# Kernel optimization log

Hardware: AMD Instinct MI355X
Metric: run time of the kernel (lower is better)

The kernel has to match this reference:

```python
import jax, jax.numpy as jnp
import numpy as np

NODES = 62        # electrodes per graph (hard-coded in model)
BATCH = 2048      # graphs per batch
N = NODES * BATCH # total nodes
IN = 128          # node feature dim (inchannel)
OUT = 62          # ChebConv out channels (hard-coded)
K = 3             # Chebyshev order (config.K)
LIN = 512         # linearsize
HC = 3            # classes (kwargs['HC'])
EPS = 1e-5        # BatchNorm eps
DEG = 4           # out-neighbors per node before symmetrization


def setup_inputs() -> dict:
    key = jax.random.key(0)
    ks = jax.random.split(key, 24)

    # Block-diagonal batched graph: same random 62-node topology per graph, offset per graph.
    rng = np.random.default_rng(0)
    src = np.repeat(np.arange(NODES), DEG)
    dst = (src + 1 + rng.integers(0, NODES - 1, size=src.shape)) % NODES  # no self-loops
    base = np.stack([np.concatenate([src, dst]), np.concatenate([dst, src])])  # [2, e] symmetric
    offs = (np.arange(BATCH) * NODES)[:, None, None]                            # [B,1,1]
    edge_index = (base[None] + offs).transpose(1, 0, 2).reshape(2, -1)          # [2, E]

    in_dims = [IN, IN + OUT, IN + 2 * OUT, IN + 3 * OUT]
    inp = {
        "x": jax.random.normal(ks[0], (N, IN), dtype=jnp.float32),
        "edge_index": jnp.asarray(edge_index, dtype=jnp.int32),
    }
    for i, d in enumerate(in_dims, start=1):
        inp[f"W{i}"] = jax.random.normal(ks[2 * i], (K, d, OUT), dtype=jnp.float32) * (1.0 / np.sqrt(d))
        inp[f"b{i}"] = jnp.zeros((OUT,), dtype=jnp.float32)
    feat = NODES * 4 * OUT  # 15376
    inp["Wh1"] = jax.random.normal(ks[10], (feat, LIN), dtype=jnp.float32) * (1.0 / np.sqrt(feat))
    inp["bh1"] = jnp.zeros((LIN,), dtype=jnp.float32)
    inp["g1"] = jnp.ones((LIN,), dtype=jnp.float32)
    inp["be1"] = jnp.zeros((LIN,), dtype=jnp.float32)
    inp["Wh2"] = jax.random.normal(ks[11], (LIN, LIN // 2), dtype=jnp.float32) * (1.0 / np.sqrt(LIN))
    inp["bh2"] = jnp.zeros((LIN // 2,), dtype=jnp.float32)
    inp["g2"] = jnp.ones((LIN // 2,), dtype=jnp.float32)
    inp["be2"] = jnp.zeros((LIN // 2,), dtype=jnp.float32)
    inp["Wh3"] = jax.random.normal(ks[12], (LIN // 2, HC), dtype=jnp.float32) * (1.0 / np.sqrt(LIN // 2))
    inp["bh3"] = jnp.zeros((HC,), dtype=jnp.float32)
    return inp


def _batchnorm(h, g, b):
    m = h.mean(axis=0)
    v = h.var(axis=0)  # biased, as torch BN training forward
    return (h - m) * jax.lax.rsqrt(v + EPS) * g + b


def reference(x, edge_index, W1, b1, W2, b2, W3, b3, W4, b4,
              Wh1, bh1, g1, be1, Wh2, bh2, g2, be2, Wh3, bh3):
    n = x.shape[0]
    row, col = edge_index[0], edge_index[1]

    # scaled Laplacian L~ = 2L/lambda_max - I = -D^{-1/2} A D^{-1/2} (sym norm, lambda_max=2)
    deg = jax.ops.segment_sum(jnp.ones(row.shape, x.dtype), row, num_segments=n)
    dinv = jnp.where(deg > 0, jnp.where(deg > 0, deg, 1.0) ** -0.5, 0.0)
    w = -(dinv[row] * dinv[col])  # [E]

    def prop(h):  # L~ @ h via edge scatter/gather
        return jax.ops.segment_sum(w[:, None] * h[col], row, num_segments=n)

    def cheb(h, W, b):  # sum_k T_k(L~) h @ W_k + b
        out = h @ W[0]
        Tx0, Tx1 = h, prop(h)
        out = out + Tx1 @ W[1]
        for k in range(2, W.shape[0]):
            Tx2 = 2.0 * prop(Tx1) - Tx0
            out = out + Tx2 @ W[k]
            Tx0, Tx1 = Tx1, Tx2
        return out + b

    relu = jax.nn.relu
    x1 = relu(cheb(x, W1, b1))
    x2 = relu(cheb(jnp.concatenate([x, x1], axis=1), W2, b2))
    x3 = relu(cheb(jnp.concatenate([x, x1, x2], axis=1), W3, b3))
    x4 = relu(cheb(jnp.concatenate([x, x1, x2, x3], axis=1), W4, b4))

    feats = jnp.concatenate([x1, x2, x3, x4], axis=1)        # [N, 4*OUT]
    feats = feats.reshape(BATCH, -1)                          # [B, 62*4*OUT] (attention==identity)

    h = relu(_batchnorm(feats @ Wh1 + bh1, g1, be1))          # dropout: identity (eval)
    h = relu(_batchnorm(h @ Wh2 + bh2, g2, be2))
    logits = h @ Wh3 + bh3
    return jax.nn.softmax(logits, axis=1)
```

## Files before the change

kernel.cpp:

```cpp
#include <hip/hip_runtime.h>


#define NODES   62
#define BATCH   2048
#define NTOT    (NODES * BATCH)
#define IN_DIM  128
#define OUT_DIM 62
#define ACOLS   248
#define FEAT    15376
#define LIN1    512
#define LIN2    256
#define NCLS    3
#define BN_EPS  1e-5f

typedef __attribute__((ext_vector_type(8)))  short  short8;
typedef __attribute__((ext_vector_type(4)))  float  f32x4;
typedef __attribute__((ext_vector_type(16))) float  f32x16;
typedef __attribute__((ext_vector_type(4)))  unsigned short us4;

__device__ inline unsigned short f2bf(float x) {
    unsigned u = __builtin_bit_cast(unsigned, x);
    return (unsigned short)((u + 0x7fffu + ((u >> 16) & 1u)) >> 16);
}
__device__ inline float bf2f(unsigned short h) {
    return __builtin_bit_cast(float, (unsigned)h << 16);
}
__device__ inline void tsplit(float x, unsigned short& hi, unsigned short& lo) {
    unsigned u = __builtin_bit_cast(unsigned, x);
    hi = (unsigned short)(u >> 16);
    float r = x - __builtin_bit_cast(float, u & 0xffff0000u);
    lo = (unsigned short)(__builtin_bit_cast(unsigned, r) >> 16);
}
__device__ inline int fo(int r, int k) {
    return (((r + 2 * k) & 15) + 16 * k) * 8;
}

#define PREP_GRID 11155
__global__ __launch_bounds__(256) void prep_kernel(
    const int* __restrict__ ei, int E, int epg, unsigned short* __restrict__ Tf,
    const float* __restrict__ W1, const float* __restrict__ W2,
    const float* __restrict__ W3, const float* __restrict__ W4,
    unsigned short* __restrict__ WTall,
    const float* __restrict__ Wh1, unsigned short* __restrict__ Wh1T,
    float* __restrict__ H1, const float* __restrict__ bh1,
    float* __restrict__ H2, const float* __restrict__ bh2,
    float* __restrict__ stats)
{
    __shared__ __align__(16) char ps[48640];
    const int bid = blockIdx.x;
    const int t   = threadIdx.x;

    if (bid == 0) {
        float* Ls   = (float*)ps;
        float* Ts   = (float*)(ps + 15376);
        int*   deg  = (int*)(ps + 48144);
        float* dinv = (float*)(ps + 48392);
        for (int i = t; i < NODES * NODES; i += 256) Ls[i] = 0.f;
        if (t < NODES) deg[t] = 0;
        __syncthreads();
        const int* row = ei;
        const int* col = ei + E;
        for (int j = t; j < epg; j += 256) atomicAdd(&deg[row[j]], 1);
        __syncthreads();
        if (t < NODES) dinv[t] = (deg[t] > 0) ? rsqrtf((float)deg[t]) : 0.f;
        __syncthreads();
        for (int j = t; j < epg; j += 256) {
            int r = row[j], c = col[j];
            atomicAdd(&Ls[r * NODES + c], -dinv[r] * dinv[c]);
        }
        __syncthreads();
        for (int idx = t; idx < 4096; idx += 256) {
            int r = idx >> 6, c = idx & 63;
            float t1 = 0.f, t2 = 0.f;
            if (r < NODES && c < NODES) {
                t1 = Ls[r * NODES + c];
                float s = 0.f;
                for (int j = 0; j < NODES; ++j) s += Ls[r * NODES + j] * Ls[j * NODES + c];
                t2 = 2.f * s - (r == c ? 1.f : 0.f);
            }
            Ts[idx]        = t1;
            Ts[4096 + idx] = t2;
        }
        __syncthreads();
        for (int idx = t; idx < 16384; idx += 256) {
            int j    = idx & 7;
            int lane = (idx >> 3) & 63;
            int pl   = (idx >> 9) & 1;
            int ks   = (idx >> 10) & 3;
            int w    = (idx >> 12) & 3;
            int m = (w & 1) * 32 + (lane & 31);
            int k = ks * 16 + (lane >> 5) * 8 + j;
            float v = Ts[(w >> 1) * 4096 + m * 64 + k];
            unsigned short hi, lo;
            tsplit(v, hi, lo);
            Tf[idx] = pl ? lo : hi;
        }
    } else if (bid < 1921) {
        const int li    = bid - 1;
        const int layer = li / 480;
        const int bx    = li - layer * 480;
        const float* W = (layer == 0) ? W1 : (layer == 1) ? W2 : (layer == 2) ? W3 : W4;
        const int d    = (layer == 0) ? 128 : (layer == 1) ? 190 : (layer == 2) ? 252 : 314;
        const int dpad = (layer == 0) ? 128 : (layer == 1) ? 192 : (layer == 2) ? 256 : 320;
        const int cum  = (layer == 0) ? 0 : (layer == 1) ? 4 : (layer == 2) ? 10 : 18;
        unsigned short* WTf = WTall + (size_t)cum * 12288;
        const int total = (dpad >> 5) * 12288;
        int idx = bx * 256 + t;
        if (idx >= total) return;
        int j    = idx & 7;
        int lane = (idx >> 3) & 63;
        int f    = idx >> 9;
        int nt   = f & 1;
        int pl   = (f >> 1) & 1;
        int ks   = (f >> 2) & 1;
        int seg  = (f >> 3) % 3;
        int ch   = (f >> 3) / 3;
        int n  = nt * 32 + (lane & 31);
        int kk = ch * 32 + ks * 16 + (lane >> 5) * 8 + j;
        float v = (n < NODES && kk < d) ? W[((size_t)seg * d + kk) * OUT_DIM + n] : 0.f;
        unsigned short hi, lo;
        tsplit(v, hi, lo);
        WTf[idx] = pl ? lo : hi;
    } else if (bid < 9617) {
        const int ti = bid - 1921;
        const int k0 = (ti % 481) * 32;
        const int n0 = (ti / 481) * 32;
        float (*T)[33] = (float(*)[33])ps;
        {
            int kl = t >> 3, n4 = (t & 7) * 4;
            if (k0 + kl < FEAT) {
                float4 v = *(const float4*)&Wh1[(size_t)(k0 + kl) * LIN1 + n0 + n4];
                T[kl][n4] = v.x; T[kl][n4 + 1] = v.y; T[kl][n4 + 2] = v.z; T[kl][n4 + 3] = v.w;
            }
        }
        __syncthreads();
        {
            int nl = t >> 3, k4 = (t & 7) * 4;
            if (k0 + k4 + 3 < FEAT) {
                ushort4 o;
                o.x = f2bf(T[k4 + 0][nl]);
                o.y = f2bf(T[k4 + 1][nl]);
                o.z = f2bf(T[k4 + 2][nl]);
                o.w = f2bf(T[k4 + 3][nl]);
                *(ushort4*)&Wh1T[(size_t)(n0 + nl) * FEAT + k0 + k4] = o;
            }
        }
    } else {
        const int i = (bid - 9617) * 256 + t;
        const int n1 = BATCH * LIN1 / 4;
        const int n2 = BATCH * LIN2 / 4;
        if (i < n1) {
            ((float4*)H1)[i] = ((const float4*)bh1)[i & (LIN1 / 4 - 1)];
        } else if (i - n1 < n2) {
            int j = i - n1;
            ((float4*)H2)[j] = ((const float4*)bh2)[j & (LIN2 / 4 - 1)];
        } else {
            int j = i - n1 - n2;
            if (j < 512)
                ((float4*)stats)[j] = (float4){0.f, 0.f, 0.f, 0.f};
        }
    }
}

__global__ __launch_bounds__(256, 4) void cheb_mfma(
    const float* __restrict__ x, float* __restrict__ X248,
    const unsigned short* __restrict__ WTf, const unsigned short* __restrict__ Tf,
    const float* __restrict__ bias, int d, int dpad)
{
    __shared__ __align__(16) unsigned short smem[17408];
    __shared__ float bias_s[64];

    unsigned short* hA = smem;
    unsigned short* Bs = smem + 5120;

    const int tid  = threadIdx.x;
    const int g    = blockIdx.x;
    const int lane = tid & 63;
    const int wv   = tid >> 6;
    const int mtw  = wv >> 1, ntw = wv & 1;

    if (tid < 64) bias_s[tid] = (tid < OUT_DIM) ? bias[tid] : 0.f;

    const int srow = tid >> 2;
    const int scg  = (tid & 3) * 8;

    const int nchunk = dpad >> 5;

    f32x16 acc[3];
    #pragma unroll
    for (int s = 0; s < 3; ++s)
        #pragma unroll
        for (int i = 0; i < 16; ++i) acc[s][i] = 0.f;

    float  vh[8];
    short8 breg[6];

#define LOADCH(cn)                                                             \
    do {                                                                       \
        const int gf_ = (cn) * 32 + scg;                                       \
        if (srow < NODES) {                                                    \
            if ((cn) * 32 < IN_DIM) {                                          \
                const float4* p_ = (const float4*)&x[(size_t)(g * NODES + srow) * IN_DIM + gf_]; \
                float4 a_ = p_[0], b_ = p_[1];                                 \
                vh[0] = a_.x; vh[1] = a_.y; vh[2] = a_.z; vh[3] = a_.w;        \
                vh[4] = b_.x; vh[5] = b_.y; vh[6] = b_.z; vh[7] = b_.w;        \
            } else if (gf_ + 8 <= d) {                                         \
                const float4* p_ = (const float4*)&X248[(size_t)(g * NODES + srow) * ACOLS + (gf_ - IN_DIM)]; \
                float4 a_ = p_[0], b_ = p_[1];                                 \
                vh[0] = a_.x; vh[1] = a_.y; vh[2] = a_.z; vh[3] = a_.w;        \
                vh[4] = b_.x; vh[5] = b_.y; vh[6] = b_.z; vh[7] = b_.w;        \
            } else {                                                           \
                _Pragma("unroll")                                              \
                for (int p = 0; p < 8; ++p)                                    \
                    vh[p] = (gf_ + p < d)                                      \
                        ? X248[(size_t)(g * NODES + srow) * ACOLS + (gf_ - IN_DIM) + p] : 0.f; \
            }                                                                  \
        } else {                                                               \
            _Pragma("unroll")                                                  \
            for (int p = 0; p < 8; ++p) vh[p] = 0.f;                           \
        }                                                                      \
        const short8* wsrc_ = (const short8*)(WTf + (size_t)(cn) * 12288);     \
        _Pragma("unroll")                                                      \
        for (int i = 0; i < 6; ++i) breg[i] = wsrc_[i * 256 + tid];            \
    } while (0)

    LOADCH(0);

    for (int ch = 0; ch < nchunk; ++ch) {
        {
            short8 hi8, lo8;
            #pragma unroll
            for (int p = 0; p < 8; ++p) {
                unsigned short h_, l_;
                tsplit(vh[p], h_, l_);
                hi8[p] = (short)h_; lo8[p] = (short)l_;
            }
            *(short8*)&hA[srow * 40 + scg]        = hi8;
            *(short8*)&hA[2560 + srow * 40 + scg] = lo8;
            #pragma unroll
            for (int i = 0; i < 6; ++i) ((short8*)Bs)[i * 256 + tid] = breg[i];
        }
        __syncthreads();
        if (ch + 1 < nchunk) LOADCH(ch + 1);
        {
            const int arow = mtw * 32 + (lane & 31);
            const int akf  = (lane >> 5) * 8;
            #pragma unroll
            for (int ks = 0; ks < 2; ++ks) {
                short8 ahi = *(const short8*)&hA[arow * 40 + ks * 16 + akf];
                short8 alo = *(const short8*)&hA[2560 + arow * 40 + ks * 16 + akf];
                #pragma unroll
                for (int seg = 0; seg < 3; ++seg) {
                    const unsigned short* bp =
                        Bs + ((((seg * 2 + ks) * 2 + 0) * 2 + ntw) << 9) + lane * 8;
                    short8 bhi = *(const short8*)bp;
                    short8 blo = *(const short8*)(bp + 1024);
                    acc[seg] = __builtin_amdgcn_mfma_f32_32x32x16_bf16(ahi, bhi, acc[seg], 0, 0, 0);
                    acc[seg] = __builtin_amdgcn_mfma_f32_32x32x16_bf16(ahi, blo, acc[seg], 0, 0, 0);
                    acc[seg] = __builtin_amdgcn_mfma_f32_32x32x16_bf16(alo, bhi, acc[seg], 0, 0, 0);
                }
            }
        }
        __syncthreads();
    }
#undef LOADCH

    short8 Tr[2][4][2];
    #pragma unroll
    for (int mat = 0; mat < 2; ++mat) {
        const int w = mat * 2 + mtw;
        #pragma unroll
        for (int ks = 0; ks < 4; ++ks)
            #pragma unroll
            for (int pl = 0; pl < 2; ++pl)
                Tr[mat][ks][pl] =
                    *(const short8*)(Tf + (((size_t)(w * 4 + ks) * 2 + pl) << 9) + lane * 8);
    }
    {
        const int jb = (lane >> 5) * 4;
        const int lq = lane & 31;
        #pragma unroll
        for (int q = 0; q < 4; ++q) {
            const int ks2 = mtw * 2 + (q >> 1);
            const int lp  = lq + 32 * (q & 1);
            us4 s1h, s1l, s2h, s2l;
            #pragma unroll
            for (int r = 0; r < 4; ++r) {
                unsigned short hi_, lo_;
                tsplit(acc[1][q * 4 + r], hi_, lo_);
                s1h[r] = hi_; s1l[r] = lo_;
                tsplit(acc[2][q * 4 + r], hi_, lo_);
                s2h[r] = hi_; s2l[r] = lo_;
            }
            const int base = lp * 8 + jb;
            *(us4*)&smem[((((0 + ks2) * 2 + 0) * 2 + ntw) << 9) + base] = s1h;
            *(us4*)&smem[((((0 + ks2) * 2 + 1) * 2 + ntw) << 9) + base] = s1l;
            *(us4*)&smem[((((4 + ks2) * 2 + 0) * 2 + ntw) << 9) + base] = s2h;
            *(us4*)&smem[((((4 + ks2) * 2 + 1) * 2 + ntw) << 9) + base] = s2l;
        }
    }
    __syncthreads();
    f32x16 out = acc[0];
    #pragma unroll
    for (int mat = 0; mat < 2; ++mat)
        #pragma unroll
        for (int ks = 0; ks < 4; ++ks) {
            const unsigned short* sp =
                smem + ((((mat * 4 + ks) * 2 + 0) * 2 + ntw) << 9) + lane * 8;
            short8 shi = *(const short8*)sp;
            short8 slo = *(const short8*)(sp + 1024);
            out = __builtin_amdgcn_mfma_f32_32x32x16_bf16(Tr[mat][ks][0], shi, out, 0, 0, 0);
            out = __builtin_amdgcn_mfma_f32_32x32x16_bf16(Tr[mat][ks][0], slo, out, 0, 0, 0);
            out = __builtin_amdgcn_mfma_f32_32x32x16_bf16(Tr[mat][ks][1], shi, out, 0, 0, 0);
        }
    {
        const int c = ntw * 32 + (lane & 31);
        if (c < OUT_DIM) {
            const int mbase = mtw * 32 + 4 * (lane >> 5);
            #pragma unroll
            for (int reg = 0; reg < 16; ++reg) {
                int m = mbase + (reg & 3) + 8 * (reg >> 2);
                if (m < NODES) {
                    float v = fmaxf(out[reg] + bias_s[c], 0.f);
                    X248[(size_t)(g * NODES + m) * ACOLS + (d - IN_DIM) + c] = v;
                }
            }
        }
    }
}

#define SPLIT1 8
__global__ __launch_bounds__(256) void gemm_head1_mfma(
    const float* __restrict__ F32, const unsigned short* __restrict__ WT1,
    float* __restrict__ H1)
{
    __shared__ __align__(16) unsigned short A16[4 * 512];
    __shared__ __align__(16) unsigned short B16[8 * 512];
    const int tid  = threadIdx.x;
    const int lane = tid & 63;
    const int wv   = tid >> 6;
    const int bm = blockIdx.x, bnb = blockIdx.y, s = blockIdx.z;
    const int c0 = (481 * s) / SPLIT1, c1 = (481 * (s + 1)) / SPLIT1;
    const int mr = tid >> 2, kg = (tid & 3) * 8;
    const int mrB = tid >> 1, kgB = (tid & 1) * 16;
    const int aoff  = (mr >> 4) * 512 + fo(mr & 15, tid & 3);
    const int boff0 = (mrB >> 4) * 512 + fo(mrB & 15, (tid & 1) * 2);
    const int boff1 = (mrB >> 4) * 512 + fo(mrB & 15, (tid & 1) * 2 + 1);
    const int roff  = fo(lane & 15, lane >> 4);

    f32x4 acc[8];
    #pragma unroll
    for (int i = 0; i < 8; ++i) acc[i] = (f32x4){0.f, 0.f, 0.f, 0.f};

    float4 u0, u1;
    short8 bv0, bv1;
#define LOAD1(cn)                                                              \
    do {                                                                       \
        const int k_ = (cn) * 32 + kg;                                         \
        u0 = (float4){0.f, 0.f, 0.f, 0.f};                                     \
        u1 = (float4){0.f, 0.f, 0.f, 0.f};                                     \
        bv0 = (short8){0, 0, 0, 0, 0, 0, 0, 0};                                \
        bv1 = (short8){0, 0, 0, 0, 0, 0, 0, 0};                                \
        if (k_ + 8 <= FEAT) {                                                  \
            const float4* p_ = (const float4*)&F32[(size_t)(bm * 64 + mr) * FEAT + k_]; \
            u0 = p_[0]; u1 = p_[1];                                            \
        }                                                                      \
        const int kB_ = (cn) * 32 + kgB;                                       \
        if (kB_ + 8 <= FEAT)                                                   \
            bv0 = *(const short8*)&WT1[(size_t)(bnb * 128 + mrB) * FEAT + kB_]; \
        if (kB_ + 16 <= FEAT)                                                  \
            bv1 = *(const short8*)&WT1[(size_t)(bnb * 128 + mrB) * FEAT + kB_ + 8]; \
    } while (0)

    LOAD1(c0);
    for (int ch = c0; ch < c1; ++ch) {
        {
            short8 av;
            av[0] = (short)f2bf(u0.x); av[1] = (short)f2bf(u0.y);
            av[2] = (short)f2bf(u0.z); av[3] = (short)f2bf(u0.w);
            av[4] = (short)f2bf(u1.x); av[5] = (short)f2bf(u1.y);
            av[6] = (short)f2bf(u1.z); av[7] = (short)f2bf(u1.w);
            *(short8*)&A16[aoff]  = av;
            *(short8*)&B16[boff0] = bv0;
            *(short8*)&B16[boff1] = bv1;
        }
        __syncthreads();
        if (ch + 1 < c1) LOAD1(ch + 1);
        short8 af = *(short8*)&A16[wv * 512 + roff];
        #pragma unroll
        for (int nt = 0; nt < 8; ++nt) {
            short8 bf = *(short8*)&B16[nt * 512 + roff];
            acc[nt] = __builtin_amdgcn_mfma_f32_16x16x32_bf16(af, bf, acc[nt], 0, 0, 0);
        }
        __syncthreads();
    }
#undef LOAD1
    const int m0 = bm * 64 + wv * 16 + (lane >> 4) * 4;
    #pragma unroll
    for (int nt = 0; nt < 8; ++nt) {
        int c = bnb * 128 + nt * 16 + (lane & 15);
        #pragma unroll
        for (int rg = 0; rg < 4; ++rg)
            atomicAdd(&H1[(size_t)(m0 + rg) * LIN1 + c], acc[nt][rg]);
    }
}

__global__ __launch_bounds__(256) void bn_stats(
    const float* __restrict__ H, int C,
    float* __restrict__ Sg, float* __restrict__ S2g)
{
    const int ct = threadIdx.x & 15;
    const int rt = threadIdx.x >> 4;
    const int c  = blockIdx.x * 16 + ct;
    const int r0 = blockIdx.y * 16 + rt;
    float s = 0.f, s2 = 0.f;
    for (int r = r0; r < BATCH; r += 256) {
        float v = H[(size_t)r * C + c];
        s += v; s2 += v * v;
    }
    __shared__ float Ss[16][17], S2s[16][17];
    Ss[rt][ct] = s; S2s[rt][ct] = s2;
    __syncthreads();
    if (rt == 0) {
        float ts = 0.f, ts2 = 0.f;
        #pragma unroll
        for (int i = 0; i < 16; ++i) { ts += Ss[i][ct]; ts2 += S2s[i][ct]; }
        atomicAdd(&Sg[c], ts);
        atomicAdd(&S2g[c], ts2);
    }
}

#define ACC16(av, bv) do {                              \
    acc[0][0] = fmaf((av).x, (bv).x, acc[0][0]);        \
    acc[0][1] = fmaf((av).x, (bv).y, acc[0][1]);        \
    acc[0][2] = fmaf((av).x, (bv).z, acc[0][2]);        \
    acc[0][3] = fmaf((av).x, (bv).w, acc[0][3]);        \
    acc[1][0] = fmaf((av).y, (bv).x, acc[1][0]);        \
    acc[1][1] = fmaf((av).y, (bv).y, acc[1][1]);        \
    acc[1][2] = fmaf((av).y, (bv).z, acc[1][2]);        \
    acc[1][3] = fmaf((av).y, (bv).w, acc[1][3]);        \
    acc[2][0] = fmaf((av).z, (bv).x, acc[2][0]);        \
    acc[2][1] = fmaf((av).z, (bv).y, acc[2][1]);        \
    acc[2][2] = fmaf((av).z, (bv).z, acc[2][2]);        \
    acc[2][3] = fmaf((av).z, (bv).w, acc[2][3]);        \
    acc[3][0] = fmaf((av).w, (bv).x, acc[3][0]);        \
    acc[3][1] = fmaf((av).w, (bv).y, acc[3][1]);        \
    acc[3][2] = fmaf((av).w, (bv).z, acc[3][2]);        \
    acc[3][3] = fmaf((av).w, (bv).w, acc[3][3]);        \
} while (0)

#define SPLIT2 4
__global__ __launch_bounds__(256) void gemm2_kernel(
    const float* __restrict__ A, const float* __restrict__ B,
    float* __restrict__ C,
    const float* __restrict__ Sg1, const float* __restrict__ S2g1,
    const float* __restrict__ g1, const float* __restrict__ be1)
{
    __shared__ __align__(16) float As[16 * 72];
    __shared__ __align__(16) float Bs[16 * 64];
    __shared__ float scs[128], shs[128];
    const int bm = blockIdx.x, bnb = blockIdx.y, s = blockIdx.z;
    const int tid = threadIdx.x;
    const int ty4 = (tid >> 4) * 4;
    const int tx4 = (tid & 15) * 4;
    const int kbeg = s * (LIN1 / SPLIT2);
    const int kend = kbeg + LIN1 / SPLIT2;
    if (tid < 128) {
        const int k = kbeg + tid;
        float mn  = Sg1[k] * (1.f / BATCH);
        float var = S2g1[k] * (1.f / BATCH) - mn * mn;
        float sc  = g1[k] * rsqrtf(var + BN_EPS);
        scs[tid] = sc;
        shs[tid] = be1[k] - mn * sc;
    }
    __syncthreads();
    float acc[4][4] = {};
    for (int k0 = kbeg; k0 < kend; k0 += 16) {
        for (int i = tid; i < 1024; i += 256) {
            int m = i >> 4, kt = i & 15;
            float raw = A[(size_t)(bm * 64 + m) * LIN1 + k0 + kt];
            int kl = k0 + kt - kbeg;
            As[kt * 72 + m] = fmaxf(fmaf(raw, scs[kl], shs[kl]), 0.f);
        }
        for (int i = tid; i < 1024; i += 256) {
            int kt = i >> 6, c = i & 63;
            Bs[kt * 64 + c] = B[(size_t)(k0 + kt) * LIN2 + bnb * 64 + c];
        }
        __syncthreads();
        #pragma unroll
        for (int kt = 0; kt < 16; ++kt) {
            const float4 av = *(const float4*)&As[kt * 72 + ty4];
            const float4 bv = *(const float4*)&Bs[kt * 64 + tx4];
            ACC16(av, bv);
        }
        __syncthreads();
    }
    const int b = bm * 64 + ty4, c = bnb * 64 + tx4;
    #pragma unroll
    for (int i = 0; i < 4; ++i)
        #pragma unroll
        for (int j = 0; j < 4; ++j)
            atomicAdd(&C[(size_t)(b + i) * LIN2 + c + j], acc[i][j]);
}

__global__ __launch_bounds__(256) void final_kernel(
    const float* __restrict__ H2, const float* __restrict__ Wh3,
    const float* __restrict__ bh3, float* __restrict__ out,
    const float* __restrict__ Sg2, const float* __restrict__ S2g2,
    const float* __restrict__ g2, const float* __restrict__ be2)
{
    __shared__ float Ws[LIN2 * NCLS];
    __shared__ float bs[NCLS];
    __shared__ float sc2[LIN2], sh2[LIN2];
    const int tid = threadIdx.x;
    for (int i = tid; i < LIN2 * NCLS; i += 256) Ws[i] = Wh3[i];
    if (tid < NCLS) bs[tid] = bh3[tid];
    {
        float mn  = Sg2[tid] * (1.f / BATCH);
        float var = S2g2[tid] * (1.f / BATCH) - mn * mn;
        float sc  = g2[tid] * rsqrtf(var + BN_EPS);
        sc2[tid] = sc;
        sh2[tid] = be2[tid] - mn * sc;
    }
    __syncthreads();
    const int r     = blockIdx.x * 32 + (tid >> 3);
    const int lane8 = tid & 7;
    float a0 = (lane8 == 0) ? bs[0] : 0.f;
    float a1 = (lane8 == 0) ? bs[1] : 0.f;
    float a2 = (lane8 == 0) ? bs[2] : 0.f;
    const float4* row = (const float4*)&H2[(size_t)r * LIN2];
    #pragma unroll
    for (int i = 0; i < 8; ++i) {
        const int k4 = lane8 + i * 8;
        float4 h = row[k4];
        const int k = k4 * 4;
        float h0 = fmaxf(fmaf(h.x, sc2[k + 0], sh2[k + 0]), 0.f);
        float h1 = fmaxf(fmaf(h.y, sc2[k + 1], sh2[k + 1]), 0.f);
        float h2v = fmaxf(fmaf(h.z, sc2[k + 2], sh2[k + 2]), 0.f);
        float h3 = fmaxf(fmaf(h.w, sc2[k + 3], sh2[k + 3]), 0.f);
        a0 = fmaf(h0, Ws[(k + 0) * 3 + 0], a0);
        a1 = fmaf(h0, Ws[(k + 0) * 3 + 1], a1);
        a2 = fmaf(h0, Ws[(k + 0) * 3 + 2], a2);
        a0 = fmaf(h1, Ws[(k + 1) * 3 + 0], a0);
        a1 = fmaf(h1, Ws[(k + 1) * 3 + 1], a1);
        a2 = fmaf(h1, Ws[(k + 1) * 3 + 2], a2);
        a0 = fmaf(h2v, Ws[(k + 2) * 3 + 0], a0);
        a1 = fmaf(h2v, Ws[(k + 2) * 3 + 1], a1);
        a2 = fmaf(h2v, Ws[(k + 2) * 3 + 2], a2);
        a0 = fmaf(h3, Ws[(k + 3) * 3 + 0], a0);
        a1 = fmaf(h3, Ws[(k + 3) * 3 + 1], a1);
        a2 = fmaf(h3, Ws[(k + 3) * 3 + 2], a2);
    }
    #pragma unroll
    for (int m = 1; m < 8; m <<= 1) {
        a0 += __shfl_xor(a0, m);
        a1 += __shfl_xor(a1, m);
        a2 += __shfl_xor(a2, m);
    }
    if (lane8 == 0) {
        float mx = fmaxf(a0, fmaxf(a1, a2));
        float e0 = expf(a0 - mx), e1 = expf(a1 - mx), e2 = expf(a2 - mx);
        float inv = 1.f / (e0 + e1 + e2);
        out[r * 3 + 0] = e0 * inv;
        out[r * 3 + 1] = e1 * inv;
        out[r * 3 + 2] = e2 * inv;
    }
}

extern "C" void kernel_launch(void* const* d_in, const int* in_sizes, int n_in,
                              void* d_out, int out_size, void* d_ws, size_t ws_size,
                              hipStream_t stream)
{
    const float* x   = (const float*)d_in[0];
    const int*   ei  = (const int*)  d_in[1];
    const float* W1  = (const float*)d_in[2];
    const float* b1  = (const float*)d_in[3];
    const float* W2  = (const float*)d_in[4];
    const float* b2  = (const float*)d_in[5];
    const float* W3  = (const float*)d_in[6];
    const float* b3  = (const float*)d_in[7];
    const float* W4  = (const float*)d_in[8];
    const float* b4  = (const float*)d_in[9];
    const float* Wh1 = (const float*)d_in[10];
    const float* bh1 = (const float*)d_in[11];
    const float* g1  = (const float*)d_in[12];
    const float* be1 = (const float*)d_in[13];
    const float* Wh2 = (const float*)d_in[14];
    const float* bh2 = (const float*)d_in[15];
    const float* g2  = (const float*)d_in[16];
    const float* be2 = (const float*)d_in[17];
    const float* Wh3 = (const float*)d_in[18];
    const float* bh3 = (const float*)d_in[19];
    float* out = (float*)d_out;

    char* ws = (char*)d_ws;
    float* Sg1  = (float*)(ws + 0);
    float* S2g1 = (float*)(ws + 2048);
    float* Sg2  = (float*)(ws + 4096);
    float* S2g2 = (float*)(ws + 5120);
    unsigned short* Tf    = (unsigned short*)(ws + 32768);
    unsigned short* WTall = (unsigned short*)(ws + 65536);
    unsigned short* Wh1T  = (unsigned short*)(ws + 753664);
    float* X248 = (float*)(ws + 16498688);
    float* H1   = (float*)(ws + 142458880);
    float* H2   = (float*)(ws + 146653184);

    const int E   = in_sizes[1] / 2;
    const int epg = E / BATCH;

    prep_kernel<<<PREP_GRID, 256, 0, stream>>>(
        ei, E, epg, Tf, W1, W2, W3, W4, WTall, Wh1, Wh1T, H1, bh1, H2, bh2,
        (float*)ws);

    cheb_mfma<<<BATCH, 256, 0, stream>>>(x, X248, WTall + (size_t)0 * 12288,  Tf, b1, 128, 128);
    cheb_mfma<<<BATCH, 256, 0, stream>>>(x, X248, WTall + (size_t)4 * 12288,  Tf, b2, 190, 192);
    cheb_mfma<<<BATCH, 256, 0, stream>>>(x, X248, WTall + (size_t)10 * 12288, Tf, b3, 252, 256);
    cheb_mfma<<<BATCH, 256, 0, stream>>>(x, X248, WTall + (size_t)18 * 12288, Tf, b4, 314, 320);

    gemm_head1_mfma<<<dim3(32, 4, SPLIT1), 256, 0, stream>>>(X248, Wh1T, H1);

    bn_stats<<<dim3(LIN1 / 16, 16), 256, 0, stream>>>(H1, LIN1, Sg1, S2g1);
    gemm2_kernel<<<dim3(32, 4, SPLIT2), 256, 0, stream>>>(H1, Wh2, H2, Sg1, S2g1, g1, be1);
    bn_stats<<<dim3(LIN2 / 16, 16), 256, 0, stream>>>(H2, LIN2, Sg2, S2g2);
    final_kernel<<<BATCH / 32, 256, 0, stream>>>(H2, Wh3, bh3, out, Sg2, S2g2, g2, be2);
}
```

Baseline: 518.8 us.

## Store Cheb outputs as pre-split bf16 hi/lo and fold head prep into layer-1 launch

Cheb layer outputs are now stored as bf16 hi/lo pairs (round-to-nearest split) instead of fp32. Later layers therefore load pre-split values without re-splitting, and the head GEMM reads the bf16 hi half directly with no per-chunk conversion. The Wh1 transpose/convert and H1/H2/stats initialisation move out of the prep kernel into extra blocks of the first cheb launch, so they overlap with layer-1 compute. This trades extra index arithmetic and a changed rounding scheme for less memory traffic and less conversion work.

```diff
diff --git a/kernel.cpp b/kernel.cpp
--- a/kernel.cpp
+++ b/kernel.cpp
@@ -8,6 +8,7 @@
 #define OUT_DIM 62
 #define ACOLS   248
 #define FEAT    15376
+#define GSTR    30752
 #define LIN1    512
 #define LIN2    256
 #define NCLS    3
@@ -31,20 +32,20 @@
     float r = x - __builtin_bit_cast(float, u & 0xffff0000u);
     lo = (unsigned short)(__builtin_bit_cast(unsigned, r) >> 16);
 }
+__device__ inline void rsplit(float x, unsigned short& hi, unsigned short& lo) {
+    hi = f2bf(x);
+    lo = f2bf(x - bf2f(hi));
+}
 __device__ inline int fo(int r, int k) {
     return (((r + 2 * k) & 15) + 16 * k) * 8;
 }
 
-#define PREP_GRID 11155
-__global__ __launch_bounds__(256) void prep_kernel(
+#define PREPC_GRID 1921
+__global__ __launch_bounds__(256) void prep_core(
     const int* __restrict__ ei, int E, int epg, unsigned short* __restrict__ Tf,
     const float* __restrict__ W1, const float* __restrict__ W2,
     const float* __restrict__ W3, const float* __restrict__ W4,
-    unsigned short* __restrict__ WTall,
-    const float* __restrict__ Wh1, unsigned short* __restrict__ Wh1T,
-    float* __restrict__ H1, const float* __restrict__ bh1,
-    float* __restrict__ H2, const float* __restrict__ bh2,
-    float* __restrict__ stats)
+    unsigned short* __restrict__ WTall)
 {
     __shared__ __align__(16) char ps[48640];
     const int bid = blockIdx.x;
@@ -95,7 +96,7 @@
             tsplit(v, hi, lo);
             Tf[idx] = pl ? lo : hi;
         }
-    } else if (bid < 1921) {
+    } else {
         const int li    = bid - 1;
         const int layer = li / 480;
         const int bx    = li - layer * 480;
@@ -121,60 +122,71 @@
         unsigned short hi, lo;
         tsplit(v, hi, lo);
         WTf[idx] = pl ? lo : hi;
-    } else if (bid < 9617) {
-        const int ti = bid - 1921;
-        const int k0 = (ti % 481) * 32;
-        const int n0 = (ti / 481) * 32;
-        float (*T)[33] = (float(*)[33])ps;
-        {
-            int kl = t >> 3, n4 = (t & 7) * 4;
-            if (k0 + kl < FEAT) {
-                float4 v = *(const float4*)&Wh1[(size_t)(k0 + kl) * LIN1 + n0 + n4];
-                T[kl][n4] = v.x; T[kl][n4 + 1] = v.y; T[kl][n4 + 2] = v.z; T[kl][n4 + 3] = v.w;
-            }
-        }
-        __syncthreads();
-        {
-            int nl = t >> 3, k4 = (t & 7) * 4;
-            if (k0 + k4 + 3 < FEAT) {
-                ushort4 o;
-                o.x = f2bf(T[k4 + 0][nl]);
-                o.y = f2bf(T[k4 + 1][nl]);
-                o.z = f2bf(T[k4 + 2][nl]);
-                o.w = f2bf(T[k4 + 3][nl]);
-                *(ushort4*)&Wh1T[(size_t)(n0 + nl) * FEAT + k0 + k4] = o;
-            }
-        }
-    } else {
-        const int i = (bid - 9617) * 256 + t;
-        const int n1 = BATCH * LIN1 / 4;
-        const int n2 = BATCH * LIN2 / 4;
-        if (i < n1) {
-            ((float4*)H1)[i] = ((const float4*)bh1)[i & (LIN1 / 4 - 1)];
-        } else if (i - n1 < n2) {
-            int j = i - n1;
-            ((float4*)H2)[j] = ((const float4*)bh2)[j & (LIN2 / 4 - 1)];
-        } else {
-            int j = i - n1 - n2;
-            if (j < 512)
-                ((float4*)stats)[j] = (float4){0.f, 0.f, 0.f, 0.f};
-        }
     }
 }
 
 __global__ __launch_bounds__(256, 4) void cheb_mfma(
-    const float* __restrict__ x, float* __restrict__ X248,
+    const float* __restrict__ x, unsigned short* __restrict__ Xs,
     const unsigned short* __restrict__ WTf, const unsigned short* __restrict__ Tf,
-    const float* __restrict__ bias, int d, int dpad)
+    const float* __restrict__ bias, int d, int dpad,
+    const float* __restrict__ Wh1, unsigned short* __restrict__ Wh1T,
+    float* __restrict__ H1, const float* __restrict__ bh1,
+    float* __restrict__ H2, const float* __restrict__ bh2,
+    float* __restrict__ stats)
 {
     __shared__ __align__(16) unsigned short smem[17408];
     __shared__ float bias_s[64];
 
+    const int bid = blockIdx.x;
+    const int tid = threadIdx.x;
+
+    if (bid >= BATCH) {
+        const int j = bid - BATCH;
+        if (j < 7696) {
+            const int k0 = (j % 481) * 32;
+            const int n0 = (j / 481) * 32;
+            float (*T)[33] = (float(*)[33])smem;
+            {
+                int kl = tid >> 3, n4 = (tid & 7) * 4;
+                if (k0 + kl < FEAT) {
+                    float4 v = *(const float4*)&Wh1[(size_t)(k0 + kl) * LIN1 + n0 + n4];
+                    T[kl][n4] = v.x; T[kl][n4 + 1] = v.y; T[kl][n4 + 2] = v.z; T[kl][n4 + 3] = v.w;
+                }
+            }
+            __syncthreads();
+            {
+                int nl = tid >> 3, k4 = (tid & 7) * 4;
+                if (k0 + k4 + 3 < FEAT) {
+                    ushort4 o;
+                    o.x = f2bf(T[k4 + 0][nl]);
+                    o.y = f2bf(T[k4 + 1][nl]);
+                    o.z = f2bf(T[k4 + 2][nl]);
+                    o.w = f2bf(T[k4 + 3][nl]);
+                    *(ushort4*)&Wh1T[(size_t)(n0 + nl) * FEAT + k0 + k4] = o;
+                }
+            }
+        } else {
+            const int i = (j - 7696) * 256 + tid;
+            const int n1 = BATCH * LIN1 / 4;
+            const int n2 = BATCH * LIN2 / 4;
+            if (i < n1) {
+                ((float4*)H1)[i] = ((const float4*)bh1)[i & (LIN1 / 4 - 1)];
+            } else if (i - n1 < n2) {
+                int jj = i - n1;
+                ((float4*)H2)[jj] = ((const float4*)bh2)[jj & (LIN2 / 4 - 1)];
+            } else {
+                int jj = i - n1 - n2;
+                if (jj < 512)
+                    ((float4*)stats)[jj] = (float4){0.f, 0.f, 0.f, 0.f};
+            }
+        }
+        return;
+    }
+
     unsigned short* hA = smem;
     unsigned short* Bs = smem + 5120;
 
-    const int tid  = threadIdx.x;
-    const int g    = blockIdx.x;
+    const int g    = bid;
     const int lane = tid & 63;
     const int wv   = tid >> 6;
     const int mtw  = wv >> 1, ntw = wv & 1;
@@ -183,6 +195,7 @@
 
     const int srow = tid >> 2;
     const int scg  = (tid & 3) * 8;
+    const size_t xbh = (size_t)g * GSTR + (size_t)srow * ACOLS;
 
     const int nchunk = dpad >> 5;
 
@@ -193,31 +206,37 @@
         for (int i = 0; i < 16; ++i) acc[s][i] = 0.f;
 
     float  vh[8];
+    short8 hv, lv;
     short8 breg[6];
 
 #define LOADCH(cn)                                                             \
     do {                                                                       \
         const int gf_ = (cn) * 32 + scg;                                       \
         if (srow < NODES) {                                                    \
-            if ((cn) * 32 < IN_DIM) {                                          \
+            if ((cn) < 4) {                                                    \
                 const float4* p_ = (const float4*)&x[(size_t)(g * NODES + srow) * IN_DIM + gf_]; \
                 float4 a_ = p_[0], b_ = p_[1];                                 \
                 vh[0] = a_.x; vh[1] = a_.y; vh[2] = a_.z; vh[3] = a_.w;        \
                 vh[4] = b_.x; vh[5] = b_.y; vh[6] = b_.z; vh[7] = b_.w;        \
             } else if (gf_ + 8 <= d) {                                         \
-                const float4* p_ = (const float4*)&X248[(size_t)(g * NODES + srow) * ACOLS + (gf_ - IN_DIM)]; \
-                float4 a_ = p_[0], b_ = p_[1];                                 \
-                vh[0] = a_.x; vh[1] = a_.y; vh[2] = a_.z; vh[3] = a_.w;        \
-                vh[4] = b_.x; vh[5] = b_.y; vh[6] = b_.z; vh[7] = b_.w;        \
+                hv = *(const short8*)&Xs[xbh + (gf_ - IN_DIM)];                \
+                lv = *(const short8*)&Xs[xbh + FEAT + (gf_ - IN_DIM)];         \
             } else {                                                           \
                 _Pragma("unroll")                                              \
-                for (int p = 0; p < 8; ++p)                                    \
-                    vh[p] = (gf_ + p < d)                                      \
-                        ? X248[(size_t)(g * NODES + srow) * ACOLS + (gf_ - IN_DIM) + p] : 0.f; \
+                for (int p = 0; p < 8; ++p) {                                  \
+                    const int gfp = gf_ + p;                                   \
+                    hv[p] = (gfp < d) ? (short)Xs[xbh + (gfp - IN_DIM)] : (short)0; \
+                    lv[p] = (gfp < d) ? (short)Xs[xbh + FEAT + (gfp - IN_DIM)] : (short)0; \
+                }                                                              \
             }                                                                  \
         } else {                                                               \
-            _Pragma("unroll")                                                  \
-            for (int p = 0; p < 8; ++p) vh[p] = 0.f;                           \
+            if ((cn) < 4) {                                                    \
+                _Pragma("unroll")                                              \
+                for (int p = 0; p < 8; ++p) vh[p] = 0.f;                       \
+            } else {                                                           \
+                hv = (short8){0, 0, 0, 0, 0, 0, 0, 0};                         \
+                lv = (short8){0, 0, 0, 0, 0, 0, 0, 0};                         \
+            }                                                                  \
         }                                                                      \
         const short8* wsrc_ = (const short8*)(WTf + (size_t)(cn) * 12288);     \
         _Pragma("unroll")                                                      \
@@ -229,11 +248,15 @@
     for (int ch = 0; ch < nchunk; ++ch) {
         {
             short8 hi8, lo8;
-            #pragma unroll
-            for (int p = 0; p < 8; ++p) {
-                unsigned short h_, l_;
-                tsplit(vh[p], h_, l_);
-                hi8[p] = (short)h_; lo8[p] = (short)l_;
+            if (ch < 4) {
+                #pragma unroll
+                for (int p = 0; p < 8; ++p) {
+                    unsigned short h_, l_;
+                    rsplit(vh[p], h_, l_);
+                    hi8[p] = (short)h_; lo8[p] = (short)l_;
+                }
+            } else {
+                hi8 = hv; lo8 = lv;
             }
             *(short8*)&hA[srow * 40 + scg]        = hi8;
             *(short8*)&hA[2560 + srow * 40 + scg] = lo8;
@@ -300,7 +323,7 @@
         }
     }
     __syncthreads();
-    f32x16 out = acc[0];
+    f32x16 outv = acc[0];
     #pragma unroll
     for (int mat = 0; mat < 2; ++mat)
         #pragma unroll
@@ -309,9 +332,9 @@
                 smem + ((((mat * 4 + ks) * 2 + 0) * 2 + ntw) << 9) + lane * 8;
             short8 shi = *(const short8*)sp;
             short8 slo = *(const short8*)(sp + 1024);
-            out = __builtin_amdgcn_mfma_f32_32x32x16_bf16(Tr[mat][ks][0], shi, out, 0, 0, 0);
-            out = __builtin_amdgcn_mfma_f32_32x32x16_bf16(Tr[mat][ks][0], slo, out, 0, 0, 0);
-            out = __builtin_amdgcn_mfma_f32_32x32x16_bf16(Tr[mat][ks][1], shi, out, 0, 0, 0);
+            outv = __builtin_amdgcn_mfma_f32_32x32x16_bf16(Tr[mat][ks][0], shi, outv, 0, 0, 0);
+            outv = __builtin_amdgcn_mfma_f32_32x32x16_bf16(Tr[mat][ks][0], slo, outv, 0, 0, 0);
+            outv = __builtin_amdgcn_mfma_f32_32x32x16_bf16(Tr[mat][ks][1], shi, outv, 0, 0, 0);
         }
     {
         const int c = ntw * 32 + (lane & 31);
@@ -321,8 +344,12 @@
             for (int reg = 0; reg < 16; ++reg) {
                 int m = mbase + (reg & 3) + 8 * (reg >> 2);
                 if (m < NODES) {
-                    float v = fmaxf(out[reg] + bias_s[c], 0.f);
-                    X248[(size_t)(g * NODES + m) * ACOLS + (d - IN_DIM) + c] = v;
+                    float v = fmaxf(outv[reg] + bias_s[c], 0.f);
+                    unsigned short h_, l_;
+                    rsplit(v, h_, l_);
+                    const size_t o = (size_t)g * GSTR + (size_t)m * ACOLS + (d - IN_DIM) + c;
+                    Xs[o]        = h_;
+                    Xs[o + FEAT] = l_;
                 }
             }
         }
@@ -331,7 +358,7 @@
 
 #define SPLIT1 8
 __global__ __launch_bounds__(256) void gemm_head1_mfma(
-    const float* __restrict__ F32, const unsigned short* __restrict__ WT1,
+    const unsigned short* __restrict__ Xs, const unsigned short* __restrict__ WT1,
     float* __restrict__ H1)
 {
     __shared__ __align__(16) unsigned short A16[4 * 512];
@@ -347,24 +374,21 @@
     const int boff0 = (mrB >> 4) * 512 + fo(mrB & 15, (tid & 1) * 2);
     const int boff1 = (mrB >> 4) * 512 + fo(mrB & 15, (tid & 1) * 2 + 1);
     const int roff  = fo(lane & 15, lane >> 4);
+    const unsigned short* arow = Xs + (size_t)(bm * 64 + mr) * GSTR;
 
     f32x4 acc[8];
     #pragma unroll
     for (int i = 0; i < 8; ++i) acc[i] = (f32x4){0.f, 0.f, 0.f, 0.f};
 
-    float4 u0, u1;
-    short8 bv0, bv1;
+    short8 av, bv0, bv1;
 #define LOAD1(cn)                                                              \
     do {                                                                       \
         const int k_ = (cn) * 32 + kg;                                         \
-        u0 = (float4){0.f, 0.f, 0.f, 0.f};                                     \
-        u1 = (float4){0.f, 0.f, 0.f, 0.f};                                     \
+        av  = (short8){0, 0, 0, 0, 0, 0, 0, 0};                                \
         bv0 = (short8){0, 0, 0, 0, 0, 0, 0, 0};                                \
         bv1 = (short8){0, 0, 0, 0, 0, 0, 0, 0};                                \
-        if (k_ + 8 <= FEAT) {                                                  \
-            const float4* p_ = (const float4*)&F32[(size_t)(bm * 64 + mr) * FEAT + k_]; \
-            u0 = p_[0]; u1 = p_[1];                                            \
-        }                                                                      \
+        if (k_ + 8 <= FEAT)                                                    \
+            av = *(const short8*)(arow + k_);                                  \
         const int kB_ = (cn) * 32 + kgB;                                       \
         if (kB_ + 8 <= FEAT)                                                   \
             bv0 = *(const short8*)&WT1[(size_t)(bnb * 128 + mrB) * FEAT + kB_]; \
@@ -375,11 +399,6 @@
     LOAD1(c0);
     for (int ch = c0; ch < c1; ++ch) {
         {
-            short8 av;
-            av[0] = (short)f2bf(u0.x); av[1] = (short)f2bf(u0.y);
-            av[2] = (short)f2bf(u0.z); av[3] = (short)f2bf(u0.w);
-            av[4] = (short)f2bf(u1.x); av[5] = (short)f2bf(u1.y);
-            av[6] = (short)f2bf(u1.z); av[7] = (short)f2bf(u1.w);
             *(short8*)&A16[aoff]  = av;
             *(short8*)&B16[boff0] = bv0;
             *(short8*)&B16[boff1] = bv1;
@@ -601,23 +620,29 @@
     unsigned short* Tf    = (unsigned short*)(ws + 32768);
     unsigned short* WTall = (unsigned short*)(ws + 65536);
     unsigned short* Wh1T  = (unsigned short*)(ws + 753664);
-    float* X248 = (float*)(ws + 16498688);
+    unsigned short* Xs    = (unsigned short*)(ws + 16498688);
     float* H1   = (float*)(ws + 142458880);
     float* H2   = (float*)(ws + 146653184);
 
     const int E   = in_sizes[1] / 2;
     const int epg = E / BATCH;
 
-    prep_kernel<<<PREP_GRID, 256, 0, stream>>>(
-        ei, E, epg, Tf, W1, W2, W3, W4, WTall, Wh1, Wh1T, H1, bh1, H2, bh2,
-        (float*)ws);
-
-    cheb_mfma<<<BATCH, 256, 0, stream>>>(x, X248, WTall + (size_t)0 * 12288,  Tf, b1, 128, 128);
-    cheb_mfma<<<BATCH, 256, 0, stream>>>(x, X248, WTall + (size_t)4 * 12288,  Tf, b2, 190, 192);
-    cheb_mfma<<<BATCH, 256, 0, stream>>>(x, X248, WTall + (size_t)10 * 12288, Tf, b3, 252, 256);
-    cheb_mfma<<<BATCH, 256, 0, stream>>>(x, X248, WTall + (size_t)18 * 12288, Tf, b4, 314, 320);
-
-    gemm_head1_mfma<<<dim3(32, 4, SPLIT1), 256, 0, stream>>>(X248, Wh1T, H1);
+    prep_core<<<PREPC_GRID, 256, 0, stream>>>(ei, E, epg, Tf, W1, W2, W3, W4, WTall);
+
+    cheb_mfma<<<BATCH + 9234, 256, 0, stream>>>(
+        x, Xs, WTall + (size_t)0 * 12288, Tf, b1, 128, 128,
+        Wh1, Wh1T, H1, bh1, H2, bh2, (float*)ws);
+    cheb_mfma<<<BATCH, 256, 0, stream>>>(
+        x, Xs, WTall + (size_t)4 * 12288, Tf, b2, 190, 192,
+        Wh1, Wh1T, H1, bh1, H2, bh2, (float*)ws);
+    cheb_mfma<<<BATCH, 256, 0, stream>>>(
+        x, Xs, WTall + (size_t)10 * 12288, Tf, b3, 252, 256,
+        Wh1, Wh1T, H1, bh1, H2, bh2, (float*)ws);
+    cheb_mfma<<<BATCH, 256, 0, stream>>>(
+        x, Xs, WTall + (size_t)18 * 12288, Tf, b4, 314, 320,
+        Wh1, Wh1T, H1, bh1, H2, bh2, (float*)ws);
+
+    gemm_head1_mfma<<<dim3(32, 4, SPLIT1), 256, 0, stream>>>(Xs, Wh1T, H1);
 
     bn_stats<<<dim3(LIN1 / 16, 16), 256, 0, stream>>>(H1, LIN1, Sg1, S2g1);
     gemm2_kernel<<<dim3(32, 4, SPLIT2), 256, 0, stream>>>(H1, Wh2, H2, Sg1, S2g1, g1, be1);
```

After: 549.3 us. 5.9% more time.
